# Optimization experiments

Hardware: AMD Instinct MI355X
Metric: run time of the kernel (lower is better)

Reference implementation:

```python
import jax, jax.numpy as jnp
import numpy as np

SUBSPACE_DIMS = np.array([1, 3, 3, 1])  # grade dims of 3D Clifford algebra (8 blades)
NUM_FEAT, NUM_HEADS, N_TOKENS, BS, C = 16, 8, 2048, 4, 8


def mv_linear(x, w, b):
    # x: [B, in, 8]; w: [out, in, 4] -> repeat over subspace dims -> [out, in, 8]
    wfull = jnp.repeat(w, SUBSPACE_DIMS, axis=-1)
    out = jnp.einsum('bic,oic->boc', x, wfull)
    return out.at[:, :, 0].add(b)  # bias on scalar blade only


def setup_inputs() -> dict:
    key = jax.random.key(0)
    ks = jax.random.split(key, 9)
    s = 0.05
    return {
        'feature_matrix': jax.random.normal(ks[0], (BS * N_TOKENS, NUM_FEAT, C), jnp.float32),
        'attention_mask': jnp.zeros((BS, N_TOKENS, N_TOKENS), jnp.float32),
        'wq': jax.random.normal(ks[1], (NUM_FEAT * NUM_HEADS, NUM_FEAT, 4), jnp.float32) * s,
        'bq': jax.random.normal(ks[2], (NUM_FEAT * NUM_HEADS,), jnp.float32) * s,
        'wk': jax.random.normal(ks[3], (NUM_FEAT * NUM_HEADS, NUM_FEAT, 4), jnp.float32) * s,
        'bk': jax.random.normal(ks[4], (NUM_FEAT * NUM_HEADS,), jnp.float32) * s,
        'wv': jax.random.normal(ks[5], (NUM_FEAT * NUM_HEADS, NUM_FEAT, 4), jnp.float32) * s,
        'bv': jax.random.normal(ks[6], (NUM_FEAT * NUM_HEADS,), jnp.float32) * s,
        'wo': jax.random.normal(ks[7], (NUM_FEAT, NUM_FEAT * NUM_HEADS, 4), jnp.float32) * s,
        'bo': jax.random.normal(ks[8], (NUM_FEAT,), jnp.float32) * s,
    }


def reference(feature_matrix, attention_mask, wq, bq, wk, bk, wv, bv, wo, bo):
    H, D = NUM_HEADS, NUM_FEAT
    n = N_TOKENS
    bs = feature_matrix.shape[0] // n

    def split_heads(t):  # [(bs n), (h d), c] -> [bs, h, n, d*c]
        return t.reshape(bs, n, H, D, C).transpose(0, 2, 1, 3, 4).reshape(bs, H, n, D * C)

    q = split_heads(mv_linear(feature_matrix, wq, bq)) / jnp.sqrt(jnp.float32(D * 8))
    k = split_heads(mv_linear(feature_matrix, wk, bk))
    v = split_heads(mv_linear(feature_matrix, wv, bv))

    attn = jnp.einsum('bhqe,bhke->bhqk', q, k) + attention_mask[:, None, :, :]
    attn = jax.nn.softmax(attn, axis=-1)
    out = jnp.einsum('bhqk,bhke->bhqe', attn, v)  # [bs, H, n, D*C]

    # transpose(1,2) then view(bs*n, H*D, 8)
    out = out.transpose(0, 2, 1, 3).reshape(bs * n, H * D, C)
    return mv_linear(out, wo, bo)
```

## Files before the change

### kernel.cpp

```cpp
#include <hip/hip_runtime.h>
#include <hip/hip_bf16.h>

typedef __attribute__((ext_vector_type(8))) __bf16 bf16x8;
typedef __attribute__((ext_vector_type(4))) float f32x4;
typedef __attribute__((ext_vector_type(8))) unsigned short ushort8;

#define TOKS 8192
#define LOG2E 1.4426950408889634f

__global__ __launch_bounds__(128) void proj_kernel(
    const float* __restrict__ x,
    const float* __restrict__ wq, const float* __restrict__ bq,
    const float* __restrict__ wk, const float* __restrict__ bk,
    const float* __restrict__ wv, const float* __restrict__ bv,
    __bf16* __restrict__ Qg, __bf16* __restrict__ Kg, __bf16* __restrict__ Vg)
{
    __shared__ float xs[512];
    const int tid = threadIdx.x;
    const int t0 = blockIdx.x * 4;
    ((float4*)xs)[tid] = ((const float4*)(x + (size_t)t0 * 128))[tid];
    __syncthreads();
    const int o = tid, h = o >> 4, d = o & 15;

    float acc[3][4][8];
#pragma unroll
    for (int tz = 0; tz < 3; ++tz) {
        const float bias = (tz == 0 ? bq : tz == 1 ? bk : bv)[o];
#pragma unroll
        for (int t = 0; t < 4; ++t) {
            acc[tz][t][0] = bias;
#pragma unroll
            for (int c = 1; c < 8; ++c) acc[tz][t][c] = 0.f;
        }
    }
    const float4* w40 = (const float4*)(wq + o * 64);
    const float4* w41 = (const float4*)(wk + o * 64);
    const float4* w42 = (const float4*)(wv + o * 64);
    for (int i = 0; i < 16; ++i) {
        float4 wv3[3] = {w40[i], w41[i], w42[i]};
#pragma unroll
        for (int t = 0; t < 4; ++t) {
            f32x4 xlo = *(const f32x4*)(xs + t * 128 + i * 8);
            f32x4 xhi = *(const f32x4*)(xs + t * 128 + i * 8 + 4);
            float xv[8] = {xlo[0], xlo[1], xlo[2], xlo[3],
                           xhi[0], xhi[1], xhi[2], xhi[3]};
#pragma unroll
            for (int tz = 0; tz < 3; ++tz) {
                float wr[8] = {wv3[tz].x, wv3[tz].y, wv3[tz].y, wv3[tz].y,
                               wv3[tz].z, wv3[tz].z, wv3[tz].z, wv3[tz].w};
#pragma unroll
                for (int c = 0; c < 8; ++c) acc[tz][t][c] += xv[c] * wr[c];
            }
        }
    }
    const int bb = t0 >> 11, tt0 = t0 & 2047;
    size_t base = (((size_t)(bb * 8 + h)) * 2048 + tt0) * 128 + d * 8;
#pragma unroll
    for (int tz = 0; tz < 3; ++tz) {
        __bf16* Og = tz == 0 ? Qg : tz == 1 ? Kg : Vg;
        const float scale = (tz == 0) ? 0.08838834764831845f : 1.0f;
#pragma unroll
        for (int t = 0; t < 4; ++t) {
            bf16x8 v;
#pragma unroll
            for (int c = 0; c < 8; ++c) v[c] = (__bf16)(acc[tz][t][c] * scale);
            *(bf16x8*)(Og + base + (size_t)t * 128) = v;
        }
    }
}

__global__ __launch_bounds__(256) void transv_kernel(
    const __bf16* __restrict__ Vg, __bf16* __restrict__ Vt)
{
    __shared__ __align__(16) char T[16384];
    const int tid = threadIdx.x;
    const int bh = blockIdx.y, t0 = blockIdx.x * 64;
    const __bf16* src = Vg + ((size_t)bh * 2048 + t0) * 128;
#pragma unroll
    for (int it = 0; it < 4; ++it) {
        int cidx = it * 256 + tid;
        int r = cidx >> 4, e0 = (cidx & 15) * 8;
        bf16x8 v = *(const bf16x8*)(src + r * 128 + e0);
        *(bf16x8*)(T + ((r * 256 + e0 * 2) ^ ((r & 7) << 4))) = v;
    }
    __syncthreads();
    const int e = tid & 127, half = tid >> 7;
    __bf16* dst = Vt + ((size_t)bh * 128 + e) * 2048 + t0 + half * 32;
#pragma unroll
    for (int jc = 0; jc < 4; ++jc) {
        ushort8 o8;
#pragma unroll
        for (int j = 0; j < 8; ++j) {
            int t = half * 32 + jc * 8 + j;
            o8[j] = *(const unsigned short*)(T + ((t * 256 + e * 2) ^ ((t & 7) << 4)));
        }
        *(ushort8*)(dst + jc * 8) = o8;
    }
}

__global__ __launch_bounds__(256) void flash_kernel(
    const __bf16* __restrict__ Qg, const __bf16* __restrict__ Kg,
    const __bf16* __restrict__ Vtg, const float* __restrict__ mask,
    __bf16* __restrict__ AO)
{
    __shared__ __align__(16) char Kl[16384];
    __shared__ __align__(16) char Vl[16384];
    __shared__ __align__(16) char Pl[8192];

    const int tid = threadIdx.x;
    const int lane = tid & 63, w = tid >> 6;
    const int l15 = lane & 15, lg = lane >> 4;

    const int wid = blockIdx.y * 32 + blockIdx.x;
    const int xcd = wid & 7, j = wid >> 3;
    const int bh = (xcd << 2) | (j & 3);
    const int q0 = (j >> 2) * 64;
    const int b = bh >> 3;

    int kg[4], klb[4], vg[4], vlb[4];
#pragma unroll
    for (int it = 0; it < 4; ++it) {
        int cidx = it * 256 + tid;
        int kv = cidx >> 4, c15 = cidx & 15;
        kg[it] = kv * 128 + c15 * 8;
        klb[it] = kv * 256 + ((c15 * 16) ^ ((kv & 7) << 4));
        int e = cidx >> 3, jj = cidx & 7;
        vg[it] = e * 2048 + jj * 8;
        vlb[it] = e * 128 + ((jj * 16) ^ ((e & 7) << 4));
    }
    const __bf16* kbase = Kg + (size_t)bh * 2048 * 128;
    const __bf16* vtbase = Vtg + (size_t)bh * 128 * 2048;
    const float* mbase = mask + ((size_t)b * 2048 + q0 + w * 16 + l15) * 2048;

    bf16x8 qf[4];
    {
        const __bf16* qp = Qg + ((size_t)bh * 2048 + q0 + w * 16 + l15) * 128 + lg * 8;
#pragma unroll
        for (int ks = 0; ks < 4; ++ks) qf[ks] = *(const bf16x8*)(qp + ks * 32);
    }

    f32x4 o_acc[8];
#pragma unroll
    for (int i = 0; i < 8; ++i) o_acc[i] = (f32x4){0.f, 0.f, 0.f, 0.f};
    float lacc = 0.f;
    const int pbase = w * 2048 + l15 * 128;
    const int psw = (l15 & 7) << 4;

    bf16x8 kreg[4], vreg[4];
#pragma unroll
    for (int it = 0; it < 4; ++it) {
        kreg[it] = *(const bf16x8*)(kbase + kg[it]);
        vreg[it] = *(const bf16x8*)(vtbase + vg[it]);
    }
#pragma unroll
    for (int it = 0; it < 4; ++it) {
        *(bf16x8*)(Kl + klb[it]) = kreg[it];
        *(bf16x8*)(Vl + vlb[it]) = vreg[it];
    }
    f32x4 mr[4];
#pragma unroll
    for (int ct = 0; ct < 4; ++ct)
        mr[ct] = *(const f32x4*)(mbase + ct * 16 + lg * 4);

    for (int kv0 = 0; kv0 < 2048; kv0 += 64) {
        __syncthreads();
        const bool more = (kv0 + 64) < 2048;
        if (more) {
            const __bf16* kb = kbase + (size_t)(kv0 + 64) * 128;
            const __bf16* vb = vtbase + (kv0 + 64);
#pragma unroll
            for (int it = 0; it < 4; ++it) {
                kreg[it] = *(const bf16x8*)(kb + kg[it]);
                vreg[it] = *(const bf16x8*)(vb + vg[it]);
            }
        }

        f32x4 st[4];
        __builtin_amdgcn_s_setprio(1);
#pragma unroll
        for (int ct = 0; ct < 4; ++ct) {
            f32x4 acc = (f32x4){0.f, 0.f, 0.f, 0.f};
            const int kvr = ct * 16 + l15;
            const int rowb = kvr * 256, sw = (kvr & 7) << 4;
#pragma unroll
            for (int ks = 0; ks < 4; ++ks) {
                bf16x8 kf = *(const bf16x8*)(Kl + rowb + ((ks * 64 + lg * 16) ^ sw));
                acc = __builtin_amdgcn_mfma_f32_16x16x32_bf16(kf, qf[ks], acc, 0, 0, 0);
            }
            st[ct] = acc;
        }
        __builtin_amdgcn_s_setprio(0);

#pragma unroll
        for (int ct = 0; ct < 4; ++ct) {
            union { __bf16 h[4]; unsigned long long u64; } pk;
#pragma unroll
            for (int r = 0; r < 4; ++r) {
                float p = exp2f((st[ct][r] + mr[ct][r]) * LOG2E);
                lacc += p;
                pk.h[r] = (__bf16)p;
            }
            *(unsigned long long*)(Pl + pbase + ((ct * 32 + lg * 8) ^ psw)) = pk.u64;
        }

        asm volatile("s_waitcnt lgkmcnt(0)" ::: "memory");
        __builtin_amdgcn_sched_barrier(0);

        __builtin_amdgcn_s_setprio(1);
#pragma unroll
        for (int ks2 = 0; ks2 < 2; ++ks2) {
            bf16x8 pf = *(const bf16x8*)(Pl + pbase + ((ks2 * 64 + lg * 16) ^ psw));
#pragma unroll
            for (int ct2 = 0; ct2 < 8; ++ct2) {
                const int e = ct2 * 16 + l15;
                bf16x8 vf = *(const bf16x8*)(Vl + e * 128 +
                                             ((ks2 * 64 + lg * 16) ^ ((e & 7) << 4)));
                o_acc[ct2] = __builtin_amdgcn_mfma_f32_16x16x32_bf16(vf, pf, o_acc[ct2], 0, 0, 0);
            }
        }
        __builtin_amdgcn_s_setprio(0);
        __syncthreads();

        if (more) {
#pragma unroll
            for (int it = 0; it < 4; ++it) {
                *(bf16x8*)(Kl + klb[it]) = kreg[it];
                *(bf16x8*)(Vl + vlb[it]) = vreg[it];
            }
#pragma unroll
            for (int ct = 0; ct < 4; ++ct)
                mr[ct] = *(const f32x4*)(mbase + kv0 + 64 + ct * 16 + lg * 4);
        }
    }

    float tot = lacc;
    tot += __shfl_xor(tot, 16);
    tot += __shfl_xor(tot, 32);
    const float linv = 1.0f / tot;
    const size_t tok = (size_t)b * 2048 + q0 + w * 16 + l15;
    __bf16* aop = AO + tok * 1024 + (bh & 7) * 128;
#pragma unroll
    for (int ct2 = 0; ct2 < 8; ++ct2) {
        union { __bf16 h[4]; unsigned long long u64; } ov;
#pragma unroll
        for (int r = 0; r < 4; ++r) ov.h[r] = (__bf16)(o_acc[ct2][r] * linv);
        *(unsigned long long*)(aop + ct2 * 16 + lg * 4) = ov.u64;
    }
}

__global__ __launch_bounds__(128) void outproj_kernel(
    const __bf16* __restrict__ AO, const float* __restrict__ wo,
    const float* __restrict__ bo, float* __restrict__ out)
{
    __shared__ float al[8 * 1032];
    const int tid = threadIdx.x;
    const int t0 = blockIdx.x * 8;
#pragma unroll
    for (int it = 0; it < 8; ++it) {
        bf16x8 v = *(const bf16x8*)(AO + (size_t)(t0 + it) * 1024 + tid * 8);
        f32x4 lo = {(float)v[0], (float)v[1], (float)v[2], (float)v[3]};
        f32x4 hi = {(float)v[4], (float)v[5], (float)v[6], (float)v[7]};
        *(f32x4*)(al + it * 1032 + tid * 8) = lo;
        *(f32x4*)(al + it * 1032 + tid * 8 + 4) = hi;
    }
    __syncthreads();
    const int o = tid >> 3, t = tid & 7;
    float acc[8];
    acc[0] = bo[o];
#pragma unroll
    for (int c = 1; c < 8; ++c) acc[c] = 0.f;
    const float4* w4 = (const float4*)wo + o * 128;
    for (int ii = 0; ii < 128; ++ii) {
        float4 wv = w4[ii];
        f32x4 xlo = *(const f32x4*)(al + t * 1032 + ii * 8);
        f32x4 xhi = *(const f32x4*)(al + t * 1032 + ii * 8 + 4);
        float wr[8] = {wv.x, wv.y, wv.y, wv.y, wv.z, wv.z, wv.z, wv.w};
        float xv[8] = {xlo[0], xlo[1], xlo[2], xlo[3], xhi[0], xhi[1], xhi[2], xhi[3]};
#pragma unroll
        for (int c = 0; c < 8; ++c) acc[c] += xv[c] * wr[c];
    }
    float* op = out + (size_t)(t0 + t) * 128 + o * 8;
    *(float4*)op = (float4){acc[0], acc[1], acc[2], acc[3]};
    *(float4*)(op + 4) = (float4){acc[4], acc[5], acc[6], acc[7]};
}

extern "C" void kernel_launch(void* const* d_in, const int* in_sizes, int n_in,
                              void* d_out, int out_size, void* d_ws, size_t ws_size,
                              hipStream_t stream)
{
    const float* x    = (const float*)d_in[0];
    const float* mask = (const float*)d_in[1];
    const float* wq   = (const float*)d_in[2];
    const float* bq   = (const float*)d_in[3];
    const float* wk   = (const float*)d_in[4];
    const float* bk   = (const float*)d_in[5];
    const float* wv   = (const float*)d_in[6];
    const float* bv   = (const float*)d_in[7];
    const float* wo   = (const float*)d_in[8];
    const float* bo   = (const float*)d_in[9];
    float* out = (float*)d_out;

    const size_t SLOT = (size_t)32 * 2048 * 128;
    const size_t need = SLOT * 4 * 2;
    if (ws_size < need) {
        hipMemsetAsync(d_out, 0, (size_t)out_size * sizeof(float), stream);
        return;
    }
    __bf16* Qg = (__bf16*)d_ws;
    __bf16* Kg = Qg + SLOT;
    __bf16* Vg = Kg + SLOT;
    __bf16* Vt = Vg + SLOT;
    __bf16* AO = Vg;

    proj_kernel<<<TOKS / 4, 128, 0, stream>>>(x, wq, bq, wk, bk, wv, bv, Qg, Kg, Vg);
    transv_kernel<<<dim3(32, 32), 256, 0, stream>>>(Vg, Vt);
    flash_kernel<<<dim3(32, 32), 256, 0, stream>>>(Qg, Kg, Vt, mask, AO);
    outproj_kernel<<<TOKS / 8, 128, 0, stream>>>(AO, wo, bo, out);
}
```

Before: 197.6 us.

## Load V fragments directly from global into registers and double-buffer K in LDS

V tiles are no longer staged through shared memory: each lane loads its MFMA B-operand fragments for the current KV tile straight from global memory into registers at the top of the loop. K shared memory is double-buffered, which removes the second __syncthreads per iteration. This frees LDS bandwidth and a barrier, but puts global load latency for V on the current iteration's critical path and raises register pressure by sixteen extra 8-wide vectors.

After: 386.4 us. 1.96x slower.

```diff
diff --git a/kernel.cpp b/kernel.cpp
--- a/kernel.cpp
+++ b/kernel.cpp
@@ -103,8 +103,7 @@
     const __bf16* __restrict__ Vtg, const float* __restrict__ mask,
     __bf16* __restrict__ AO)
 {
-    __shared__ __align__(16) char Kl[16384];
-    __shared__ __align__(16) char Vl[16384];
+    __shared__ __align__(16) char Kl[2][16384];
     __shared__ __align__(16) char Pl[8192];
 
     const int tid = threadIdx.x;
@@ -117,20 +116,18 @@
     const int q0 = (j >> 2) * 64;
     const int b = bh >> 3;
 
-    int kg[4], klb[4], vg[4], vlb[4];
+    int kg[4], klb[4];
 #pragma unroll
     for (int it = 0; it < 4; ++it) {
         int cidx = it * 256 + tid;
         int kv = cidx >> 4, c15 = cidx & 15;
         kg[it] = kv * 128 + c15 * 8;
         klb[it] = kv * 256 + ((c15 * 16) ^ ((kv & 7) << 4));
-        int e = cidx >> 3, jj = cidx & 7;
-        vg[it] = e * 2048 + jj * 8;
-        vlb[it] = e * 128 + ((jj * 16) ^ ((e & 7) << 4));
     }
     const __bf16* kbase = Kg + (size_t)bh * 2048 * 128;
     const __bf16* vtbase = Vtg + (size_t)bh * 128 * 2048;
     const float* mbase = mask + ((size_t)b * 2048 + q0 + w * 16 + l15) * 2048;
+    const __bf16* vlane = vtbase + (size_t)l15 * 2048 + lg * 8;
 
     bf16x8 qf[4];
     {
@@ -146,34 +143,34 @@
     const int pbase = w * 2048 + l15 * 128;
     const int psw = (l15 & 7) << 4;
 
-    bf16x8 kreg[4], vreg[4];
-#pragma unroll
-    for (int it = 0; it < 4; ++it) {
-        kreg[it] = *(const bf16x8*)(kbase + kg[it]);
-        vreg[it] = *(const bf16x8*)(vtbase + vg[it]);
-    }
-#pragma unroll
-    for (int it = 0; it < 4; ++it) {
-        *(bf16x8*)(Kl + klb[it]) = kreg[it];
-        *(bf16x8*)(Vl + vlb[it]) = vreg[it];
-    }
+    bf16x8 kreg[4];
+#pragma unroll
+    for (int it = 0; it < 4; ++it) kreg[it] = *(const bf16x8*)(kbase + kg[it]);
+#pragma unroll
+    for (int it = 0; it < 4; ++it) *(bf16x8*)(Kl[0] + klb[it]) = kreg[it];
     f32x4 mr[4];
 #pragma unroll
     for (int ct = 0; ct < 4; ++ct)
         mr[ct] = *(const f32x4*)(mbase + ct * 16 + lg * 4);
 
+    int cur = 0;
     for (int kv0 = 0; kv0 < 2048; kv0 += 64) {
         __syncthreads();
         const bool more = (kv0 + 64) < 2048;
+
+        const __bf16* vln = vlane + kv0;
+        bf16x8 vfrag[16];
+#pragma unroll
+        for (int ct2 = 0; ct2 < 8; ++ct2) {
+            vfrag[ct2 * 2]     = *(const bf16x8*)(vln + ct2 * 32768);
+            vfrag[ct2 * 2 + 1] = *(const bf16x8*)(vln + ct2 * 32768 + 32);
+        }
         if (more) {
             const __bf16* kb = kbase + (size_t)(kv0 + 64) * 128;
-            const __bf16* vb = vtbase + (kv0 + 64);
-#pragma unroll
-            for (int it = 0; it < 4; ++it) {
-                kreg[it] = *(const bf16x8*)(kb + kg[it]);
-                vreg[it] = *(const bf16x8*)(vb + vg[it]);
-            }
-        }
+#pragma unroll
+            for (int it = 0; it < 4; ++it) kreg[it] = *(const bf16x8*)(kb + kg[it]);
+        }
+        __builtin_amdgcn_sched_barrier(0);
 
         f32x4 st[4];
         __builtin_amdgcn_s_setprio(1);
@@ -184,7 +181,7 @@
             const int rowb = kvr * 256, sw = (kvr & 7) << 4;
 #pragma unroll
             for (int ks = 0; ks < 4; ++ks) {
-                bf16x8 kf = *(const bf16x8*)(Kl + rowb + ((ks * 64 + lg * 16) ^ sw));
+                bf16x8 kf = *(const bf16x8*)(Kl[cur] + rowb + ((ks * 64 + lg * 16) ^ sw));
                 acc = __builtin_amdgcn_mfma_f32_16x16x32_bf16(kf, qf[ks], acc, 0, 0, 0);
             }
             st[ct] = acc;
@@ -212,25 +209,20 @@
             bf16x8 pf = *(const bf16x8*)(Pl + pbase + ((ks2 * 64 + lg * 16) ^ psw));
 #pragma unroll
             for (int ct2 = 0; ct2 < 8; ++ct2) {
-                const int e = ct2 * 16 + l15;
-                bf16x8 vf = *(const bf16x8*)(Vl + e * 128 +
-                                             ((ks2 * 64 + lg * 16) ^ ((e & 7) << 4)));
-                o_acc[ct2] = __builtin_amdgcn_mfma_f32_16x16x32_bf16(vf, pf, o_acc[ct2], 0, 0, 0);
+                o_acc[ct2] = __builtin_amdgcn_mfma_f32_16x16x32_bf16(
+                    vfrag[ct2 * 2 + ks2], pf, o_acc[ct2], 0, 0, 0);
             }
         }
         __builtin_amdgcn_s_setprio(0);
-        __syncthreads();
 
         if (more) {
 #pragma unroll
-            for (int it = 0; it < 4; ++it) {
-                *(bf16x8*)(Kl + klb[it]) = kreg[it];
-                *(bf16x8*)(Vl + vlb[it]) = vreg[it];
-            }
+            for (int it = 0; it < 4; ++it) *(bf16x8*)(Kl[cur ^ 1] + klb[it]) = kreg[it];
 #pragma unroll
             for (int ct = 0; ct < 4; ++ct)
                 mr[ct] = *(const f32x4*)(mbase + kv0 + 64 + ct * 16 + lg * 4);
         }
+        cur ^= 1;
     }
 
     float tot = lacc;
```
